# Performance work log

Hardware: AMD Instinct MI355X
Metric: run time of the kernel (lower is better)

## Reference

```python
import jax, jax.numpy as jnp
import numpy as np

NUM_EXPERTS = 16
TOP_K = 2
HIDDEN = 1024
INTER = 2048
NUM_TOKENS = 4096
# expert capacity: ceil(num_tokens*top_k/E * 1.5); generous so drops are negligible
CAPACITY = 768


def setup_inputs() -> dict:
    key = jax.random.key(0)
    k1, k2, k3, k4 = jax.random.split(key, 4)
    hidden_states = jax.random.normal(k1, (NUM_TOKENS, HIDDEN), dtype=jnp.float32)
    router_logits = jax.random.normal(k2, (NUM_TOKENS, NUM_EXPERTS), dtype=jnp.float32)
    # fused gate+up projection: (E, 2*I, H) laid out as [w3; w1]
    w3_w1_weight = jax.random.normal(k3, (NUM_EXPERTS, 2 * INTER, HIDDEN), dtype=jnp.float32) * 0.02
    # down projection: (E, H, I)
    w2_weight = jax.random.normal(k4, (NUM_EXPERTS, HIDDEN, INTER), dtype=jnp.float32) * 0.02
    return {
        "hidden_states": hidden_states,
        "router_logits": router_logits,
        "w3_w1_weight": w3_w1_weight,
        "w2_weight": w2_weight,
    }


def reference(hidden_states, router_logits, w3_w1_weight, w2_weight):
    N, H = hidden_states.shape
    E = w3_w1_weight.shape[0]
    I = w3_w1_weight.shape[1] // 2

    # --- routing: softmax -> top-k -> renormalize selected scales ---
    probs = jax.nn.softmax(router_logits, axis=-1)                      # (N, E)
    scales, sel = jax.lax.top_k(probs, TOP_K)                           # (N, K)
    scales = scales / jnp.sum(scales, axis=-1, keepdims=True)

    # --- dispatch: scatter (token, k) rows into per-expert capacity buffers ---
    flat_sel = sel.reshape(-1)                                          # (N*K,) int32
    flat_scale = scales.reshape(-1)                                     # (N*K,)
    onehot = jax.nn.one_hot(flat_sel, E, dtype=jnp.int32)               # (N*K, E)
    pos = jnp.cumsum(onehot, axis=0) - 1                                # running count per expert
    pos = jnp.take_along_axis(pos, flat_sel[:, None], axis=1)[:, 0]     # (N*K,) slot in expert
    valid = pos < CAPACITY
    pos_c = jnp.minimum(pos, CAPACITY - 1)
    tok = jnp.repeat(jnp.arange(N), TOP_K)                              # source token for each row
    x_rows = hidden_states[tok] * valid[:, None].astype(hidden_states.dtype)
    buf = jnp.zeros((E, CAPACITY, H), hidden_states.dtype).at[flat_sel, pos_c].add(x_rows)

    # --- per-expert grouped GEMM: SwiGLU FFN ---
    h = jnp.einsum('ech,eih->eci', buf, w3_w1_weight)                   # (E, C, 2I)
    g3, g1 = h[..., :I], h[..., I:]                                     # up (w3), gate (w1)
    inter = jax.nn.silu(g1) * g3                                        # (E, C, I)
    y = jnp.einsum('eci,ehi->ech', inter, w2_weight)                    # (E, C, H)

    # --- combine: gather back per (token, k) row, weight, and sum over k ---
    rows = y[flat_sel, pos_c] * (flat_scale * valid.astype(flat_scale.dtype))[:, None]
    out = rows.reshape(N, TOP_K, H).sum(axis=1)                         # (N, H)
    return out
```

## Files before the change

kernel.cpp:

```cpp
#include <hip/hip_runtime.h>
#include <stdint.h>

#define NUM_EXPERTS 16
#define TOP_K 2
#define HIDDEN 1024
#define INTER 2048
#define NUM_TOKENS 4096
#define CAPACITY 768
#define NFLAT (NUM_TOKENS*TOP_K)

typedef __attribute__((ext_vector_type(4))) float f32x4;
typedef __attribute__((ext_vector_type(8))) short s16x8;

static __device__ __forceinline__ unsigned short f2bf(float f){
  union { float f; unsigned int u; } v; v.f = f;
  unsigned int r = (v.u + 0x7fffu + ((v.u >> 16) & 1u)) >> 16;
  return (unsigned short)r;
}
static __device__ __forceinline__ float bf2f(unsigned short s){
  union { unsigned int u; float f; } v; v.u = ((unsigned int)s) << 16;
  return v.f;
}

__global__ void route_topk(const float* __restrict__ logits,
                           int* __restrict__ sel, float* __restrict__ scl){
  int t = blockIdx.x*blockDim.x + threadIdx.x;
  if(t >= NUM_TOKENS) return;
  const float* L = logits + (size_t)t*NUM_EXPERTS;
  float l[NUM_EXPERTS];
  #pragma unroll
  for(int j=0;j<NUM_EXPERTS;j+=4){
    float4 v = *(const float4*)(L + j);
    l[j]=v.x; l[j+1]=v.y; l[j+2]=v.z; l[j+3]=v.w;
  }
  int i1 = 0; float m1 = l[0];
  #pragma unroll
  for(int j=1;j<NUM_EXPERTS;j++) if(l[j] > m1){ m1=l[j]; i1=j; }
  int i2 = -1; float m2 = -1e30f;
  #pragma unroll
  for(int j=0;j<NUM_EXPERTS;j++) if(j != i1 && l[j] > m2){ m2=l[j]; i2=j; }
  float e  = __expf(m2 - m1);
  float s1 = 1.f/(1.f + e);
  float s2 = e*s1;
  sel[TOP_K*t]   = i1; sel[TOP_K*t+1] = i2;
  scl[TOP_K*t]   = s1; scl[TOP_K*t+1] = s2;
}

__global__ void assign_pos(const int* __restrict__ sel,
                           int* __restrict__ pos, int* __restrict__ cnt){
  const int e = blockIdx.x;
  const int tid = threadIdx.x;
  const int lane = tid & 63, w = tid >> 6;
  __shared__ int wsum[4];
  __shared__ int carry;
  if(tid == 0) carry = 0;
  __syncthreads();
  for(int c = 0; c < NFLAT; c += 256){
    int i = c + tid;
    bool flag = (sel[i] == e);
    unsigned long long mask = __ballot(flag);
    int lp   = __popcll(mask & ((1ull << lane) - 1ull));
    int wtot = __popcll(mask);
    if(lane == 0) wsum[w] = wtot;
    __syncthreads();
    int base = carry;
    int off = base;
    for(int q=0;q<w;q++) off += wsum[q];
    int tot = wsum[0] + wsum[1] + wsum[2] + wsum[3];
    if(flag) pos[i] = off + lp;
    __syncthreads();
    if(tid == 0) carry = base + tot;
  }
  if(tid == 0) cnt[e] = (carry < CAPACITY) ? carry : CAPACITY;
}

__global__ void scatter_rows(const float* __restrict__ hs,
                             const int* __restrict__ sel, const int* __restrict__ pos,
                             unsigned short* __restrict__ Abuf){
  int i = blockIdx.x*(blockDim.x>>6) + (threadIdx.x>>6);
  int lane = threadIdx.x & 63;
  if(i >= NFLAT) return;
  int p = pos[i];
  if(p >= CAPACITY) return;
  int e = sel[i];
  int tok = i >> 1;
  const float4* src = (const float4*)(hs + (size_t)tok*HIDDEN);
  unsigned short* dst = Abuf + ((size_t)e*CAPACITY + p)*HIDDEN;
  #pragma unroll
  for(int c=0;c<4;c++){
    float4 v = src[c*64 + lane];
    ushort4 o; o.x=f2bf(v.x); o.y=f2bf(v.y); o.z=f2bf(v.z); o.w=f2bf(v.w);
    *(ushort4*)(dst + (size_t)(c*64 + lane)*4) = o;
  }
}

template<int DUAL>
__global__ __launch_bounds__(256,2) void moe_gemm(
    const unsigned short* __restrict__ Abase, int lda,
    const float* __restrict__ Wbase, int ldw, int nW,
    unsigned short* __restrict__ Obase, int ldo,
    const int* __restrict__ cnts, int K)
{
  extern __shared__ char smem[];
  char* sAc  = smem;
  char* sBc  = smem + 16384;
  char* sB2c = smem + 32768;

  const int e   = blockIdx.z;
  const int cnt = cnts[e];
  const int m0  = blockIdx.y * 128;
  if(m0 >= cnt) return;
  const int n0  = blockIdx.x * 128;

  const int tid  = threadIdx.x;
  const int lane = tid & 63;
  const int w    = tid >> 6;
  const int wm   = w >> 1, wn = w & 1;

  const unsigned short* Aexp = Abase + (size_t)e*CAPACITY*lda;
  const float* W0 = Wbase + (size_t)e*nW*ldw;

  f32x4 acc[4][4];
  f32x4 acc2[4][4];
  #pragma unroll
  for(int a=0;a<4;a++)
    #pragma unroll
    for(int b=0;b<4;b++){ acc[a][b]=(f32x4)(0.f); acc2[a][b]=(f32x4)(0.f); }

  const int ar = lane >> 3;
  const int ac = (lane & 7) ^ ar;
  const int brr = tid >> 4;
  const int bcc = tid & 15;

  for(int k0 = 0; k0 < K; k0 += 64){
    #pragma unroll
    for(int q=0;q<4;q++){
      int rowbase = w*32 + q*8;
      const unsigned short* g = Aexp + (size_t)(m0 + rowbase + ar)*lda + k0 + ac*8;
      __builtin_amdgcn_global_load_lds(
          (const __attribute__((address_space(1))) void*)g,
          (__attribute__((address_space(3))) void*)(sAc + rowbase*128),
          16, 0, 0);
    }
    #pragma unroll
    for(int j=0;j<8;j++){
      int row = j*16 + brr;
      const float* gp = W0 + (size_t)(n0 + row)*ldw + k0 + bcc*4;
      float4 v = *(const float4*)gp;
      ushort4 o; o.x=f2bf(v.x); o.y=f2bf(v.y); o.z=f2bf(v.z); o.w=f2bf(v.w);
      int sb = row*128 + ((bcc*8) ^ ((row & 7) << 4));
      *(ushort4*)(sBc + sb) = o;
      if(DUAL){
        float4 v2 = *(const float4*)(gp + (size_t)INTER*ldw);
        ushort4 o2; o2.x=f2bf(v2.x); o2.y=f2bf(v2.y); o2.z=f2bf(v2.z); o2.w=f2bf(v2.w);
        *(ushort4*)(sB2c + sb) = o2;
      }
    }
    __syncthreads();
    #pragma unroll
    for(int kk=0;kk<2;kk++){
      const int kb = kk*64 + (lane >> 4)*16;
      s16x8 af[4];
      #pragma unroll
      for(int mi=0;mi<4;mi++){
        int row = wm*64 + mi*16 + (lane & 15);
        af[mi] = *(const s16x8*)(sAc + row*128 + (kb ^ ((row & 7) << 4)));
      }
      #pragma unroll
      for(int ni=0;ni<4;ni++){
        int row = wn*64 + ni*16 + (lane & 15);
        s16x8 bfr = *(const s16x8*)(sBc + row*128 + (kb ^ ((row & 7) << 4)));
        s16x8 b2r;
        if(DUAL) b2r = *(const s16x8*)(sB2c + row*128 + (kb ^ ((row & 7) << 4)));
        #pragma unroll
        for(int mi=0;mi<4;mi++){
          acc[mi][ni] = __builtin_amdgcn_mfma_f32_16x16x32_bf16(af[mi], bfr, acc[mi][ni], 0, 0, 0);
          if(DUAL)
            acc2[mi][ni] = __builtin_amdgcn_mfma_f32_16x16x32_bf16(af[mi], b2r, acc2[mi][ni], 0, 0, 0);
        }
      }
    }
    __syncthreads();
  }

  #pragma unroll
  for(int mi=0;mi<4;mi++){
    #pragma unroll
    for(int ni=0;ni<4;ni++){
      #pragma unroll
      for(int j=0;j<4;j++){
        int s = m0 + wm*64 + mi*16 + (lane >> 4)*4 + j;
        int c = n0 + wn*64 + ni*16 + (lane & 15);
        float val;
        if(DUAL){
          float g3 = acc[mi][ni][j];
          float g1 = acc2[mi][ni][j];
          val = (g1 / (1.f + __expf(-g1))) * g3;
        } else {
          val = acc[mi][ni][j];
        }
        Obase[((size_t)e*CAPACITY + s)*ldo + c] = f2bf(val);
      }
    }
  }
}

__global__ void gather_out(const unsigned short* __restrict__ Y,
                           const int* __restrict__ sel, const int* __restrict__ pos,
                           const float* __restrict__ scl, float* __restrict__ out){
  int t = blockIdx.x*(blockDim.x>>6) + (threadIdx.x>>6);
  int lane = threadIdx.x & 63;
  if(t >= NUM_TOKENS) return;
  float a[16];
  #pragma unroll
  for(int j=0;j<16;j++) a[j] = 0.f;
  #pragma unroll
  for(int k=0;k<TOP_K;k++){
    int i = TOP_K*t + k;
    int p = pos[i];
    if(p >= CAPACITY) continue;
    int e = sel[i];
    float sc = scl[i];
    const unsigned short* y = Y + ((size_t)e*CAPACITY + p)*HIDDEN;
    #pragma unroll
    for(int c=0;c<4;c++){
      ushort4 v = *(const ushort4*)(y + (size_t)(c*64 + lane)*4);
      a[c*4+0] += sc*bf2f(v.x);
      a[c*4+1] += sc*bf2f(v.y);
      a[c*4+2] += sc*bf2f(v.z);
      a[c*4+3] += sc*bf2f(v.w);
    }
  }
  float* o = out + (size_t)t*HIDDEN;
  #pragma unroll
  for(int c=0;c<4;c++){
    float4 v; v.x=a[c*4+0]; v.y=a[c*4+1]; v.z=a[c*4+2]; v.w=a[c*4+3];
    *(float4*)(o + (size_t)(c*64 + lane)*4) = v;
  }
}

extern "C" void kernel_launch(void* const* d_in, const int* in_sizes, int n_in,
                              void* d_out, int out_size, void* d_ws, size_t ws_size,
                              hipStream_t stream){
  const float* hs  = (const float*)d_in[0];
  const float* lg  = (const float*)d_in[1];
  const float* w31 = (const float*)d_in[2];
  const float* w2  = (const float*)d_in[3];
  float* out = (float*)d_out;

  char* ws = (char*)d_ws;
  int*   sel = (int*)(ws);
  float* scl = (float*)(ws + 32768);
  int*   pos = (int*)(ws + 65536);
  int*   cnt = (int*)(ws + 98304);
  unsigned short* Abuf = (unsigned short*)(ws + 131072);
  unsigned short* Ibuf = (unsigned short*)(ws + 131072 + 25165824);
  unsigned short* Ybuf = (unsigned short*)(ws + 131072 + 25165824 + 50331648);

  route_topk <<<NUM_TOKENS/256, 256, 0, stream>>>(lg, sel, scl);
  assign_pos <<<NUM_EXPERTS,    256, 0, stream>>>(sel, pos, cnt);
  scatter_rows<<<NFLAT/4,       256, 0, stream>>>(hs, sel, pos, Abuf);

  moe_gemm<1><<<dim3(INTER/128, CAPACITY/128, NUM_EXPERTS), 256, 49152, stream>>>(
      Abuf, HIDDEN, w31, HIDDEN, 2*INTER, Ibuf, INTER, cnt, HIDDEN);
  moe_gemm<0><<<dim3(HIDDEN/128, CAPACITY/128, NUM_EXPERTS), 256, 32768, stream>>>(
      Ibuf, INTER, w2, INTER, HIDDEN, Ybuf, HIDDEN, cnt, INTER);

  gather_out <<<NUM_TOKENS/4, 256, 0, stream>>>(Ybuf, sel, pos, scl, out);
}
```

Baseline: 995.5 us.

## Pre-convert expert weights to bf16 and stream them via direct-to-LDS loads

Result: faster. 842.7 us (-15.4%).

```diff
diff --git a/kernel.cpp b/kernel.cpp
--- a/kernel.cpp
+++ b/kernel.cpp
@@ -94,10 +94,25 @@
   }
 }
 
+__global__ void convert_w(const float* __restrict__ src,
+                          unsigned short* __restrict__ dst, int n8){
+  int i = blockIdx.x*blockDim.x + threadIdx.x;
+  int stride = gridDim.x*blockDim.x;
+  for(; i < n8; i += stride){
+    const float4* s = (const float4*)(src + (size_t)i*8);
+    float4 a = s[0], b = s[1];
+    ushort4 o0, o1;
+    o0.x=f2bf(a.x); o0.y=f2bf(a.y); o0.z=f2bf(a.z); o0.w=f2bf(a.w);
+    o1.x=f2bf(b.x); o1.y=f2bf(b.y); o1.z=f2bf(b.z); o1.w=f2bf(b.w);
+    ushort4* d = (ushort4*)(dst + (size_t)i*8);
+    d[0]=o0; d[1]=o1;
+  }
+}
+
 template<int DUAL>
-__global__ __launch_bounds__(256,2) void moe_gemm(
+__global__ __launch_bounds__(256,3) void moe_gemm(
     const unsigned short* __restrict__ Abase, int lda,
-    const float* __restrict__ Wbase, int ldw, int nW,
+    const unsigned short* __restrict__ Wbase, int ldw, int nW,
     unsigned short* __restrict__ Obase, int ldo,
     const int* __restrict__ cnts, int K)
 {
@@ -118,7 +133,7 @@
   const int wm   = w >> 1, wn = w & 1;
 
   const unsigned short* Aexp = Abase + (size_t)e*CAPACITY*lda;
-  const float* W0 = Wbase + (size_t)e*nW*ldw;
+  const unsigned short* Wexp = Wbase + (size_t)e*nW*ldw;
 
   f32x4 acc[4][4];
   f32x4 acc2[4][4];
@@ -129,31 +144,24 @@
 
   const int ar = lane >> 3;
   const int ac = (lane & 7) ^ ar;
-  const int brr = tid >> 4;
-  const int bcc = tid & 15;
 
   for(int k0 = 0; k0 < K; k0 += 64){
     #pragma unroll
     for(int q=0;q<4;q++){
-      int rowbase = w*32 + q*8;
-      const unsigned short* g = Aexp + (size_t)(m0 + rowbase + ar)*lda + k0 + ac*8;
+      const int rowbase = w*32 + q*8;
+      const unsigned short* gA = Aexp + (size_t)(m0 + rowbase + ar)*lda + k0 + ac*8;
       __builtin_amdgcn_global_load_lds(
-          (const __attribute__((address_space(1))) void*)g,
-          (__attribute__((address_space(3))) void*)(sAc + rowbase*128),
-          16, 0, 0);
-    }
-    #pragma unroll
-    for(int j=0;j<8;j++){
-      int row = j*16 + brr;
-      const float* gp = W0 + (size_t)(n0 + row)*ldw + k0 + bcc*4;
-      float4 v = *(const float4*)gp;
-      ushort4 o; o.x=f2bf(v.x); o.y=f2bf(v.y); o.z=f2bf(v.z); o.w=f2bf(v.w);
-      int sb = row*128 + ((bcc*8) ^ ((row & 7) << 4));
-      *(ushort4*)(sBc + sb) = o;
+          (const __attribute__((address_space(1))) void*)gA,
+          (__attribute__((address_space(3))) void*)(sAc + rowbase*128), 16, 0, 0);
+      const unsigned short* gB = Wexp + (size_t)(n0 + rowbase + ar)*ldw + k0 + ac*8;
+      __builtin_amdgcn_global_load_lds(
+          (const __attribute__((address_space(1))) void*)gB,
+          (__attribute__((address_space(3))) void*)(sBc + rowbase*128), 16, 0, 0);
       if(DUAL){
-        float4 v2 = *(const float4*)(gp + (size_t)INTER*ldw);
-        ushort4 o2; o2.x=f2bf(v2.x); o2.y=f2bf(v2.y); o2.z=f2bf(v2.z); o2.w=f2bf(v2.w);
-        *(ushort4*)(sB2c + sb) = o2;
+        const unsigned short* gB2 = gB + (size_t)INTER*ldw;
+        __builtin_amdgcn_global_load_lds(
+            (const __attribute__((address_space(1))) void*)gB2,
+            (__attribute__((address_space(3))) void*)(sB2c + rowbase*128), 16, 0, 0);
       }
     }
     __syncthreads();
@@ -253,18 +261,26 @@
   float* scl = (float*)(ws + 32768);
   int*   pos = (int*)(ws + 65536);
   int*   cnt = (int*)(ws + 98304);
-  unsigned short* Abuf = (unsigned short*)(ws + 131072);
-  unsigned short* Ibuf = (unsigned short*)(ws + 131072 + 25165824);
-  unsigned short* Ybuf = (unsigned short*)(ws + 131072 + 25165824 + 50331648);
+  unsigned short* Abuf  = (unsigned short*)(ws + 131072);
+  unsigned short* Ibuf  = (unsigned short*)(ws + 131072 + 25165824);
+  char*           big   = ws + 131072 + 25165824 + 50331648;
+  unsigned short* Wbuf1 = (unsigned short*)big;
+  unsigned short* Wbuf2 = (unsigned short*)big;
+  unsigned short* Ybuf  = (unsigned short*)(big + 67108864);
 
   route_topk <<<NUM_TOKENS/256, 256, 0, stream>>>(lg, sel, scl);
   assign_pos <<<NUM_EXPERTS,    256, 0, stream>>>(sel, pos, cnt);
   scatter_rows<<<NFLAT/4,       256, 0, stream>>>(hs, sel, pos, Abuf);
 
+  convert_w<<<2048, 256, 0, stream>>>(w31, Wbuf1, NUM_EXPERTS*2*INTER*HIDDEN/8);
+
   moe_gemm<1><<<dim3(INTER/128, CAPACITY/128, NUM_EXPERTS), 256, 49152, stream>>>(
-      Abuf, HIDDEN, w31, HIDDEN, 2*INTER, Ibuf, INTER, cnt, HIDDEN);
+      Abuf, HIDDEN, Wbuf1, HIDDEN, 2*INTER, Ibuf, INTER, cnt, HIDDEN);
+
+  convert_w<<<2048, 256, 0, stream>>>(w2, Wbuf2, NUM_EXPERTS*HIDDEN*INTER/8);
+
   moe_gemm<0><<<dim3(HIDDEN/128, CAPACITY/128, NUM_EXPERTS), 256, 32768, stream>>>(
-      Ibuf, INTER, w2, INTER, HIDDEN, Ybuf, HIDDEN, cnt, INTER);
+      Ibuf, INTER, Wbuf2, INTER, HIDDEN, Ybuf, HIDDEN, cnt, INTER);
 
   gather_out <<<NUM_TOKENS/4, 256, 0, stream>>>(Ybuf, sel, pos, scl, out);
 }
```
